# Performance work log

Hardware: AMD Instinct MI355X
Metric: run time of the kernel (lower is better)

The kernel has to match this reference:

```python
import jax, jax.numpy as jnp
import numpy as np

L, B, I, H = 1024, 128, 256, 512

def setup_inputs() -> dict:
    key = jax.random.key(0)
    k1, k2, k3, k4, k5 = jax.random.split(key, 5)
    s_i = 1.0 / np.sqrt(I)
    s_h = 1.0 / np.sqrt(H)
    return {
        "x": jax.random.normal(k1, (L, B, I), dtype=jnp.float32),
        "h": jax.random.normal(k2, (B, H), dtype=jnp.float32),
        "Wx": jax.random.uniform(k3, (H, I), jnp.float32, -s_i, s_i),
        "Wh": jax.random.uniform(k4, (H, H), jnp.float32, -s_h, s_h),
        "bh": jax.random.uniform(k5, (H,), jnp.float32, -s_h, s_h),
    }

def reference(x, h, Wx, Wh, bh):
    # Precompute input projection for all timesteps as one big GEMM:
    # (L,B,I) @ (I,H) -> (L,B,H)
    xproj = jnp.einsum("lbi,hi->lbh", x, Wx)

    def step(h_prev, xp_t):
        h_new = jnp.tanh(xp_t + h_prev @ Wh.T + bh)  # (B,H)
        return h_new, h_new

    _, h_seq = jax.lax.scan(step, h, xproj)
    return h_seq  # (L, B, H)
```

## Files before the change

### kernel.cpp

```cpp
#include <hip/hip_runtime.h>

#define L_DIM 1024
#define B_DIM 128
#define I_DIM 256
#define H_DIM 512

typedef unsigned short u16x8 __attribute__((ext_vector_type(8)));
typedef __bf16 bf16x8 __attribute__((ext_vector_type(8)));
typedef float f32x4 __attribute__((ext_vector_type(4)));
typedef unsigned long long u64;

static __device__ __forceinline__ unsigned short f2bf(float f) {
  unsigned u = __builtin_bit_cast(unsigned, f);
  u += 0x7FFFu + ((u >> 16) & 1u);
  return (unsigned short)(u >> 16);
}
static __device__ __forceinline__ float bf2f(unsigned short b) {
  return __builtin_bit_cast(float, ((unsigned)b) << 16);
}
static __device__ __forceinline__ bf16x8 ld_frag_g(const unsigned short* p, size_t idx8) {
  return __builtin_bit_cast(bf16x8, reinterpret_cast<const u16x8*>(p)[idx8]);
}

__global__ void pack_weights(const float* __restrict__ Wx, const float* __restrict__ Wh,
                             unsigned short* __restrict__ WxHi, unsigned short* __restrict__ WxLo,
                             unsigned short* __restrict__ WhHi, unsigned short* __restrict__ WhLo) {
  int tid = blockIdx.x * blockDim.x + threadIdx.x;
  if (tid < 32 * 8 * 64) {
    int lane = tid & 63, kt = (tid >> 6) & 7, nt = tid >> 9;
    int n = nt * 16 + (lane & 15), k0 = kt * 32 + (lane >> 4) * 8;
    const float* src = Wx + (size_t)n * I_DIM + k0;
    #pragma unroll
    for (int j = 0; j < 8; ++j) {
      float v = src[j];
      unsigned short hb = f2bf(v);
      WxHi[(size_t)tid * 8 + j] = hb;
      WxLo[(size_t)tid * 8 + j] = f2bf(v - bf2f(hb));
    }
  }
  if (tid < 32 * 16 * 64) {
    int lane = tid & 63, kt = (tid >> 6) & 15, nt = tid >> 10;
    int n = nt * 16 + (lane & 15), k0 = kt * 32 + (lane >> 4) * 8;
    const float* src = Wh + (size_t)n * H_DIM + k0;
    #pragma unroll
    for (int j = 0; j < 8; ++j) {
      float v = src[j];
      unsigned short hb = f2bf(v);
      WhHi[(size_t)tid * 8 + j] = hb;
      WhLo[(size_t)tid * 8 + j] = f2bf(v - bf2f(hb));
    }
  }
}

__global__ __launch_bounds__(256) void xproj_kernel(const float* __restrict__ x,
    const unsigned short* __restrict__ WxHi, const unsigned short* __restrict__ WxLo,
    const float* __restrict__ bh, float* __restrict__ out) {
  __shared__ unsigned short ahi[128][40];
  __shared__ unsigned short alo[128][40];
  const int tid = threadIdx.x, lane = tid & 63, wid = tid >> 6;
  const int mbase = blockIdx.x * 128, cbase = blockIdx.y * 128;
  const int wrow = (wid >> 1) * 64, wcol = (wid & 1) * 64;
  f32x4 acc[4][4] = {};
  const int srow = tid >> 1, shalf = (tid & 1) * 16;

  for (int kt = 0; kt < 8; ++kt) {
    const f32x4* src = reinterpret_cast<const f32x4*>(
        x + (size_t)(mbase + srow) * I_DIM + kt * 32 + shalf);
    f32x4 v[4];
    v[0] = src[0]; v[1] = src[1]; v[2] = src[2]; v[3] = src[3];
    u16x8 hh[2], ll[2];
    #pragma unroll
    for (int q = 0; q < 2; ++q) {
      #pragma unroll
      for (int e = 0; e < 8; ++e) {
        float f = v[q * 2 + (e >> 2)][e & 3];
        unsigned short hb = f2bf(f);
        hh[q][e] = hb;
        ll[q][e] = f2bf(f - bf2f(hb));
      }
    }
    __syncthreads();
    *reinterpret_cast<u16x8*>(&ahi[srow][shalf]) = hh[0];
    *reinterpret_cast<u16x8*>(&ahi[srow][shalf + 8]) = hh[1];
    *reinterpret_cast<u16x8*>(&alo[srow][shalf]) = ll[0];
    *reinterpret_cast<u16x8*>(&alo[srow][shalf + 8]) = ll[1];
    __syncthreads();

    bf16x8 amh[4], aml[4];
    #pragma unroll
    for (int m = 0; m < 4; ++m) {
      amh[m] = __builtin_bit_cast(bf16x8, *reinterpret_cast<const u16x8*>(
          &ahi[wrow + m * 16 + (lane & 15)][(lane >> 4) * 8]));
      aml[m] = __builtin_bit_cast(bf16x8, *reinterpret_cast<const u16x8*>(
          &alo[wrow + m * 16 + (lane & 15)][(lane >> 4) * 8]));
    }
    bf16x8 bhh[4], bll[4];
    #pragma unroll
    for (int n = 0; n < 4; ++n) {
      int ntg = (cbase + wcol) / 16 + n;
      size_t idx = (size_t)(ntg * 8 + kt) * 64 + lane;
      bhh[n] = ld_frag_g(WxHi, idx);
      bll[n] = ld_frag_g(WxLo, idx);
    }
    #pragma unroll
    for (int m = 0; m < 4; ++m) {
      #pragma unroll
      for (int n = 0; n < 4; ++n) {
        acc[m][n] = __builtin_amdgcn_mfma_f32_16x16x32_bf16(amh[m], bhh[n], acc[m][n], 0, 0, 0);
        acc[m][n] = __builtin_amdgcn_mfma_f32_16x16x32_bf16(aml[m], bhh[n], acc[m][n], 0, 0, 0);
        acc[m][n] = __builtin_amdgcn_mfma_f32_16x16x32_bf16(amh[m], bll[n], acc[m][n], 0, 0, 0);
      }
    }
  }

  #pragma unroll
  for (int n = 0; n < 4; ++n) {
    int col = cbase + wcol + n * 16 + (lane & 15);
    float bv = bh[col];
    #pragma unroll
    for (int m = 0; m < 4; ++m) {
      int rg = mbase + wrow + m * 16 + ((lane >> 4) << 2);
      #pragma unroll
      for (int r = 0; r < 4; ++r)
        out[(size_t)(rg + r) * H_DIM + col] = acc[m][n][r] + bv;
    }
  }
}

__global__ __launch_bounds__(256, 1) void rnn_kernel(const float* __restrict__ h0,
    const unsigned short* __restrict__ WhHi, const unsigned short* __restrict__ WhLo,
    unsigned int* __restrict__ tags, u64* __restrict__ gbuf,
    float* __restrict__ out) {
  __shared__ unsigned short hb[16 * 520];
  const int tid = threadIdx.x, lane = tid & 63, w = tid >> 6;
  const int g = blockIdx.x & 7, c = blockIdx.x >> 3;

  bf16x8 wfh[16], wfl[16];
  #pragma unroll
  for (int kt = 0; kt < 16; ++kt) {
    size_t idx = (size_t)((c * 4 + w) * 16 + kt) * 64 + lane;
    wfh[kt] = ld_frag_g(WhHi, idx);
    wfl[kt] = ld_frag_g(WhLo, idx);
  }
  for (int i = tid; i < 1024; i += 256) {
    int row = i >> 6, col0 = (i & 63) * 8;
    const f32x4* s = reinterpret_cast<const f32x4*>(h0 + (size_t)(g * 16 + row) * H_DIM + col0);
    f32x4 v0 = s[0], v1 = s[1];
    u16x8 hv;
    #pragma unroll
    for (int e = 0; e < 4; ++e) { hv[e] = f2bf(v0[e]); hv[4 + e] = f2bf(v1[e]); }
    *reinterpret_cast<u16x8*>(&hb[row * 520 + col0]) = hv;
  }
  __syncthreads();

  const int arow = lane & 15;
  const int aoff = (lane >> 4) * 8;
  const int drow = (lane >> 4) * 4;
  const int gcol = c * 64 + w * 16 + (lane & 15);
  const int pslot = (w * 16 + (lane & 15)) * 4 + (lane >> 4);
  const int ccol = tid >> 2;
  const int crow0 = (tid & 3) * 4;

  f32x4 xpv;
  #pragma unroll
  for (int r = 0; r < 4; ++r)
    xpv[r] = out[(size_t)(g * 16 + drow + r) * H_DIM + gcol];

  for (int t = 0; t < L_DIM; ++t) {
    const size_t obase = ((size_t)t * B_DIM + g * 16) * H_DIM;

    bf16x8 af[16];
    #pragma unroll
    for (int kt = 0; kt < 16; ++kt)
      af[kt] = __builtin_bit_cast(bf16x8, *reinterpret_cast<const u16x8*>(
          &hb[arow * 520 + kt * 32 + aoff]));
    f32x4 a0 = {}, a1 = {}, a2 = {}, a3 = {};
    #pragma unroll
    for (int kt = 0; kt < 16; kt += 2) {
      a0 = __builtin_amdgcn_mfma_f32_16x16x32_bf16(af[kt], wfh[kt], a0, 0, 0, 0);
      a1 = __builtin_amdgcn_mfma_f32_16x16x32_bf16(af[kt], wfl[kt], a1, 0, 0, 0);
      a2 = __builtin_amdgcn_mfma_f32_16x16x32_bf16(af[kt + 1], wfh[kt + 1], a2, 0, 0, 0);
      a3 = __builtin_amdgcn_mfma_f32_16x16x32_bf16(af[kt + 1], wfl[kt + 1], a3, 0, 0, 0);
    }

    float hv[4]; unsigned short hu[4];
    #pragma unroll
    for (int r = 0; r < 4; ++r) {
      float z = a0[r] + a1[r] + a2[r] + a3[r] + xpv[r];
      float e = __expf(2.0f * z);
      hv[r] = 1.0f - 2.0f / (e + 1.0f);
      hu[r] = f2bf(hv[r]);
    }

    if (t < L_DIM - 1) {
      const unsigned buf = (t + 1) & 1;
      u64 pv = (u64)hu[0] | ((u64)hu[1] << 16) | ((u64)hu[2] << 32) | ((u64)hu[3] << 48);
      __hip_atomic_store(gbuf + (((size_t)(buf * 8 + g) * 8 + c) * 256 + pslot), pv,
                         __ATOMIC_RELAXED, __HIP_MEMORY_SCOPE_AGENT);
      __builtin_amdgcn_sched_barrier(0);
      asm volatile("s_waitcnt vmcnt(0)" ::: "memory");
      __builtin_amdgcn_sched_barrier(0);
      if (lane == 0)
        __hip_atomic_store(tags + ((size_t)((buf * 8 + g) * 8 + c)) * 4 + w,
                           (unsigned)(t + 1), __ATOMIC_RELAXED, __HIP_MEMORY_SCOPE_AGENT);

      #pragma unroll
      for (int r = 0; r < 4; ++r)
        out[obase + (size_t)(drow + r) * H_DIM + gcol] = hv[r];
      const size_t obn = ((size_t)(t + 1) * B_DIM + g * 16) * H_DIM;
      #pragma unroll
      for (int r = 0; r < 4; ++r)
        xpv[r] = out[obn + (size_t)(drow + r) * H_DIM + gcol];

      if (lane < 7) {
        int s = lane + (lane >= c ? 1 : 0);
        const unsigned int* tp = tags + ((size_t)((buf * 8 + g) * 8 + s)) * 4 + w;
        while (__hip_atomic_load(tp, __ATOMIC_RELAXED, __HIP_MEMORY_SCOPE_AGENT)
               < (unsigned)(t + 1)) {}
      }
      __builtin_amdgcn_sched_barrier(0);
      u64 pul[7];
      #pragma unroll
      for (int si = 0; si < 7; ++si) {
        int s = si + (si >= c ? 1 : 0);
        pul[si] = __hip_atomic_load(gbuf + (((size_t)(buf * 8 + g) * 8 + s) * 256 + tid),
                                    __ATOMIC_RELAXED, __HIP_MEMORY_SCOPE_AGENT);
      }
      __builtin_amdgcn_sched_barrier(0);
      __builtin_amdgcn_s_barrier();
      __builtin_amdgcn_sched_barrier(0);
      #pragma unroll
      for (int r = 0; r < 4; ++r)
        hb[(drow + r) * 520 + gcol] = hu[r];
      #pragma unroll
      for (int si = 0; si < 7; ++si) {
        int s = si + (si >= c ? 1 : 0);
        #pragma unroll
        for (int dr = 0; dr < 4; ++dr)
          hb[(crow0 + dr) * 520 + s * 64 + ccol] = (unsigned short)(pul[si] >> (16 * dr));
      }
      __builtin_amdgcn_sched_barrier(0);
      asm volatile("s_waitcnt lgkmcnt(0)" ::: "memory");
      __builtin_amdgcn_sched_barrier(0);
      __builtin_amdgcn_s_barrier();
      __builtin_amdgcn_sched_barrier(0);
    } else {
      #pragma unroll
      for (int r = 0; r < 4; ++r)
        out[obase + (size_t)(drow + r) * H_DIM + gcol] = hv[r];
    }
  }
}

extern "C" void kernel_launch(void* const* d_in, const int* in_sizes, int n_in,
                              void* d_out, int out_size, void* d_ws, size_t ws_size,
                              hipStream_t stream) {
  (void)in_sizes; (void)n_in; (void)out_size; (void)ws_size;
  const float* x  = (const float*)d_in[0];
  const float* h0 = (const float*)d_in[1];
  const float* Wx = (const float*)d_in[2];
  const float* Wh = (const float*)d_in[3];
  const float* bh = (const float*)d_in[4];
  float* out = (float*)d_out;

  unsigned short* WxHi = (unsigned short*)d_ws;
  unsigned short* WxLo = WxHi + 131072;
  unsigned short* WhHi = WxLo + 131072;
  unsigned short* WhLo = WhHi + 262144;
  unsigned int*   tags = (unsigned int*)((char*)d_ws + 1572864);
  u64*            gbuf = (u64*)((char*)d_ws + 1575936);

  hipMemsetAsync(tags, 0, 2048, stream);

  hipLaunchKernelGGL(pack_weights, dim3(128), dim3(256), 0, stream,
                     Wx, Wh, WxHi, WxLo, WhHi, WhLo);
  hipLaunchKernelGGL(xproj_kernel, dim3(1024, 4), dim3(256), 0, stream,
                     x, WxHi, WxLo, bh, out);
  hipLaunchKernelGGL(rnn_kernel, dim3(64), dim3(256), 0, stream,
                     h0, WhHi, WhLo, tags, gbuf, out);
}
```

Baseline: 3.002 ms.

## Embed step tags in exchanged hidden-state words and double-buffer LDS

Each step's cross-block exchange of hidden state now writes every bf16 value together with the step number in one 32-bit word. Consumers spin directly on the data words, so the separate tag array, the vmcnt drain before the flag store and the pre-write barrier are all gone. The LDS hidden-state buffer is double-buffered, so the next step's copy can be filled without waiting for the current reads to finish. In exchange, each block now reads the full 16x512 slab from global memory instead of only its peers' slices. The slab reuses the workspace region that held the packed Wx weights and relies on stale contents never matching a step tag.

Result: slower. 4.140 ms (+37.9%).

```diff
diff --git a/kernel.cpp b/kernel.cpp
--- a/kernel.cpp
+++ b/kernel.cpp
@@ -9,6 +9,7 @@
 typedef __bf16 bf16x8 __attribute__((ext_vector_type(8)));
 typedef float f32x4 __attribute__((ext_vector_type(4)));
 typedef unsigned long long u64;
+typedef unsigned int u32;
 
 static __device__ __forceinline__ unsigned short f2bf(float f) {
   unsigned u = __builtin_bit_cast(unsigned, f);
@@ -129,9 +130,8 @@
 
 __global__ __launch_bounds__(256, 1) void rnn_kernel(const float* __restrict__ h0,
     const unsigned short* __restrict__ WhHi, const unsigned short* __restrict__ WhLo,
-    unsigned int* __restrict__ tags, u64* __restrict__ gbuf,
-    float* __restrict__ out) {
-  __shared__ unsigned short hb[16 * 520];
+    u32* __restrict__ slab, float* __restrict__ out) {
+  __shared__ __attribute__((aligned(16))) unsigned short hb[2][16 * 520];
   const int tid = threadIdx.x, lane = tid & 63, w = tid >> 6;
   const int g = blockIdx.x & 7, c = blockIdx.x >> 3;
 
@@ -149,7 +149,7 @@
     u16x8 hv;
     #pragma unroll
     for (int e = 0; e < 4; ++e) { hv[e] = f2bf(v0[e]); hv[4 + e] = f2bf(v1[e]); }
-    *reinterpret_cast<u16x8*>(&hb[row * 520 + col0]) = hv;
+    *reinterpret_cast<u16x8*>(&hb[0][row * 520 + col0]) = hv;
   }
   __syncthreads();
 
@@ -157,9 +157,6 @@
   const int aoff = (lane >> 4) * 8;
   const int drow = (lane >> 4) * 4;
   const int gcol = c * 64 + w * 16 + (lane & 15);
-  const int pslot = (w * 16 + (lane & 15)) * 4 + (lane >> 4);
-  const int ccol = tid >> 2;
-  const int crow0 = (tid & 3) * 4;
 
   f32x4 xpv;
   #pragma unroll
@@ -168,12 +165,13 @@
 
   for (int t = 0; t < L_DIM; ++t) {
     const size_t obase = ((size_t)t * B_DIM + g * 16) * H_DIM;
+    const unsigned short* hbc = hb[t & 1];
 
     bf16x8 af[16];
     #pragma unroll
     for (int kt = 0; kt < 16; ++kt)
       af[kt] = __builtin_bit_cast(bf16x8, *reinterpret_cast<const u16x8*>(
-          &hb[arow * 520 + kt * 32 + aoff]));
+          &hbc[arow * 520 + kt * 32 + aoff]));
     f32x4 a0 = {}, a1 = {}, a2 = {}, a3 = {};
     #pragma unroll
     for (int kt = 0; kt < 16; kt += 2) {
@@ -193,16 +191,14 @@
     }
 
     if (t < L_DIM - 1) {
-      const unsigned buf = (t + 1) & 1;
-      u64 pv = (u64)hu[0] | ((u64)hu[1] << 16) | ((u64)hu[2] << 32) | ((u64)hu[3] << 48);
-      __hip_atomic_store(gbuf + (((size_t)(buf * 8 + g) * 8 + c) * 256 + pslot), pv,
-                         __ATOMIC_RELAXED, __HIP_MEMORY_SCOPE_AGENT);
-      __builtin_amdgcn_sched_barrier(0);
-      asm volatile("s_waitcnt vmcnt(0)" ::: "memory");
-      __builtin_amdgcn_sched_barrier(0);
-      if (lane == 0)
-        __hip_atomic_store(tags + ((size_t)((buf * 8 + g) * 8 + c)) * 4 + w,
-                           (unsigned)(t + 1), __ATOMIC_RELAXED, __HIP_MEMORY_SCOPE_AGENT);
+      const unsigned step = (unsigned)(t + 1);
+      u32* sg = slab + ((size_t)((step & 1) * 8 + g)) * 8192;
+      const unsigned cbits = step << 16;
+
+      #pragma unroll
+      for (int r = 0; r < 4; ++r)
+        __hip_atomic_store(&sg[(drow + r) * 512 + gcol], cbits | (u32)hu[r],
+                           __ATOMIC_RELAXED, __HIP_MEMORY_SCOPE_AGENT);
 
       #pragma unroll
       for (int r = 0; r < 4; ++r)
@@ -212,32 +208,25 @@
       for (int r = 0; r < 4; ++r)
         xpv[r] = out[obn + (size_t)(drow + r) * H_DIM + gcol];
 
-      if (lane < 7) {
-        int s = lane + (lane >= c ? 1 : 0);
-        const unsigned int* tp = tags + ((size_t)((buf * 8 + g) * 8 + s)) * 4 + w;
-        while (__hip_atomic_load(tp, __ATOMIC_RELAXED, __HIP_MEMORY_SCOPE_AGENT)
-               < (unsigned)(t + 1)) {}
-      }
-      __builtin_amdgcn_sched_barrier(0);
-      u64 pul[7];
-      #pragma unroll
-      for (int si = 0; si < 7; ++si) {
-        int s = si + (si >= c ? 1 : 0);
-        pul[si] = __hip_atomic_load(gbuf + (((size_t)(buf * 8 + g) * 8 + s) * 256 + tid),
+      u64* sp = reinterpret_cast<u64*>(sg);
+      u64 pv[16];
+      #pragma unroll
+      for (int row = 0; row < 16; ++row)
+        pv[row] = __hip_atomic_load(sp + row * 256 + tid,
                                     __ATOMIC_RELAXED, __HIP_MEMORY_SCOPE_AGENT);
-      }
-      __builtin_amdgcn_sched_barrier(0);
-      __builtin_amdgcn_s_barrier();
-      __builtin_amdgcn_sched_barrier(0);
-      #pragma unroll
-      for (int r = 0; r < 4; ++r)
-        hb[(drow + r) * 520 + gcol] = hu[r];
-      #pragma unroll
-      for (int si = 0; si < 7; ++si) {
-        int s = si + (si >= c ? 1 : 0);
-        #pragma unroll
-        for (int dr = 0; dr < 4; ++dr)
-          hb[(crow0 + dr) * 520 + s * 64 + ccol] = (unsigned short)(pul[si] >> (16 * dr));
+      const u64 expect = (u64)step * 0x0001000000010000ull;
+      #pragma unroll
+      for (int row = 0; row < 16; ++row) {
+        while ((pv[row] & 0xFFFF0000FFFF0000ull) != expect)
+          pv[row] = __hip_atomic_load(sp + row * 256 + tid,
+                                      __ATOMIC_RELAXED, __HIP_MEMORY_SCOPE_AGENT);
+      }
+
+      unsigned short* hbn = hb[(t + 1) & 1];
+      #pragma unroll
+      for (int row = 0; row < 16; ++row) {
+        u32 pk = (u32)(pv[row] & 0xFFFFull) | (u32)((pv[row] >> 16) & 0xFFFF0000ull);
+        *reinterpret_cast<u32*>(&hbn[row * 520 + 2 * tid]) = pk;
       }
       __builtin_amdgcn_sched_barrier(0);
       asm volatile("s_waitcnt lgkmcnt(0)" ::: "memory");
@@ -267,15 +256,12 @@
   unsigned short* WxLo = WxHi + 131072;
   unsigned short* WhHi = WxLo + 131072;
   unsigned short* WhLo = WhHi + 262144;
-  unsigned int*   tags = (unsigned int*)((char*)d_ws + 1572864);
-  u64*            gbuf = (u64*)((char*)d_ws + 1575936);
-
-  hipMemsetAsync(tags, 0, 2048, stream);
+  u32* slab = (u32*)d_ws;
 
   hipLaunchKernelGGL(pack_weights, dim3(128), dim3(256), 0, stream,
                      Wx, Wh, WxHi, WxLo, WhHi, WhLo);
   hipLaunchKernelGGL(xproj_kernel, dim3(1024, 4), dim3(256), 0, stream,
                      x, WxHi, WxLo, bh, out);
   hipLaunchKernelGGL(rnn_kernel, dim3(64), dim3(256), 0, stream,
-                     h0, WhHi, WhLo, tags, gbuf, out);
-}
+                     h0, WhHi, WhLo, slab, out);
+}
```

## Double-buffer hidden-state LDS tile to drop one barrier per timestep

Applied to the files above, without the earlier changes.

Splits the shared hidden-state buffer into two halves alternating by timestep, so new values can be written into the next buffer without first waiting for all waves to finish reading the current one. This removes one of the two workgroup barriers in each recurrent step. It also prefetches the input projection two steps ahead rather than one, to hide global load latency. In exchange it doubles LDS use and makes correctness depend on the ping-pong ordering across the remaining barrier.

Measured after the change: 2.804 ms. 6.6% less time.

```diff
diff --git a/kernel.cpp b/kernel.cpp
--- a/kernel.cpp
+++ b/kernel.cpp
@@ -9,6 +9,7 @@
 typedef __bf16 bf16x8 __attribute__((ext_vector_type(8)));
 typedef float f32x4 __attribute__((ext_vector_type(4)));
 typedef unsigned long long u64;
+typedef unsigned int u32;
 
 static __device__ __forceinline__ unsigned short f2bf(float f) {
   unsigned u = __builtin_bit_cast(unsigned, f);
@@ -131,7 +132,7 @@
     const unsigned short* __restrict__ WhHi, const unsigned short* __restrict__ WhLo,
     unsigned int* __restrict__ tags, u64* __restrict__ gbuf,
     float* __restrict__ out) {
-  __shared__ unsigned short hb[16 * 520];
+  __shared__ unsigned short hb[2][16 * 520];
   const int tid = threadIdx.x, lane = tid & 63, w = tid >> 6;
   const int g = blockIdx.x & 7, c = blockIdx.x >> 3;
 
@@ -149,7 +150,7 @@
     u16x8 hv;
     #pragma unroll
     for (int e = 0; e < 4; ++e) { hv[e] = f2bf(v0[e]); hv[4 + e] = f2bf(v1[e]); }
-    *reinterpret_cast<u16x8*>(&hb[row * 520 + col0]) = hv;
+    *reinterpret_cast<u16x8*>(&hb[0][row * 520 + col0]) = hv;
   }
   __syncthreads();
 
@@ -161,19 +162,23 @@
   const int ccol = tid >> 2;
   const int crow0 = (tid & 3) * 4;
 
-  f32x4 xpv;
+  f32x4 xpA, xpB;
   #pragma unroll
   for (int r = 0; r < 4; ++r)
-    xpv[r] = out[(size_t)(g * 16 + drow + r) * H_DIM + gcol];
+    xpA[r] = out[(size_t)(g * 16 + drow + r) * H_DIM + gcol];
+  #pragma unroll
+  for (int r = 0; r < 4; ++r)
+    xpB[r] = out[(size_t)B_DIM * H_DIM + (size_t)(g * 16 + drow + r) * H_DIM + gcol];
 
   for (int t = 0; t < L_DIM; ++t) {
     const size_t obase = ((size_t)t * B_DIM + g * 16) * H_DIM;
+    const int cur = t & 1;
 
     bf16x8 af[16];
     #pragma unroll
     for (int kt = 0; kt < 16; ++kt)
       af[kt] = __builtin_bit_cast(bf16x8, *reinterpret_cast<const u16x8*>(
-          &hb[arow * 520 + kt * 32 + aoff]));
+          &hb[cur][arow * 520 + kt * 32 + aoff]));
     f32x4 a0 = {}, a1 = {}, a2 = {}, a3 = {};
     #pragma unroll
     for (int kt = 0; kt < 16; kt += 2) {
@@ -186,69 +191,74 @@
     float hv[4]; unsigned short hu[4];
     #pragma unroll
     for (int r = 0; r < 4; ++r) {
-      float z = a0[r] + a1[r] + a2[r] + a3[r] + xpv[r];
+      float z = a0[r] + a1[r] + a2[r] + a3[r] + xpA[r];
       float e = __expf(2.0f * z);
       hv[r] = 1.0f - 2.0f / (e + 1.0f);
       hu[r] = f2bf(hv[r]);
     }
 
-    if (t < L_DIM - 1) {
-      const unsigned buf = (t + 1) & 1;
-      u64 pv = (u64)hu[0] | ((u64)hu[1] << 16) | ((u64)hu[2] << 32) | ((u64)hu[3] << 48);
-      __hip_atomic_store(gbuf + (((size_t)(buf * 8 + g) * 8 + c) * 256 + pslot), pv,
-                         __ATOMIC_RELAXED, __HIP_MEMORY_SCOPE_AGENT);
-      __builtin_amdgcn_sched_barrier(0);
-      asm volatile("s_waitcnt vmcnt(0)" ::: "memory");
-      __builtin_amdgcn_sched_barrier(0);
-      if (lane == 0)
-        __hip_atomic_store(tags + ((size_t)((buf * 8 + g) * 8 + c)) * 4 + w,
-                           (unsigned)(t + 1), __ATOMIC_RELAXED, __HIP_MEMORY_SCOPE_AGENT);
-
+    if (t == L_DIM - 1) {
       #pragma unroll
       for (int r = 0; r < 4; ++r)
         out[obase + (size_t)(drow + r) * H_DIM + gcol] = hv[r];
-      const size_t obn = ((size_t)(t + 1) * B_DIM + g * 16) * H_DIM;
+      break;
+    }
+
+    const unsigned step = (unsigned)(t + 1);
+    const unsigned buf = step & 1;
+
+    u64 pv = (u64)hu[0] | ((u64)hu[1] << 16) | ((u64)hu[2] << 32) | ((u64)hu[3] << 48);
+    __hip_atomic_store(gbuf + (((size_t)(buf * 8 + g) * 8 + c) * 256 + pslot), pv,
+                       __ATOMIC_RELAXED, __HIP_MEMORY_SCOPE_AGENT);
+    __builtin_amdgcn_sched_barrier(0);
+    asm volatile("s_waitcnt vmcnt(0)" ::: "memory");
+    __builtin_amdgcn_sched_barrier(0);
+    if (lane == 0)
+      __hip_atomic_store(tags + ((size_t)((buf * 8 + g) * 8 + c)) * 4 + w,
+                         step, __ATOMIC_RELAXED, __HIP_MEMORY_SCOPE_AGENT);
+
+    #pragma unroll
+    for (int r = 0; r < 4; ++r)
+      hb[buf][(drow + r) * 520 + gcol] = hu[r];
+
+    #pragma unroll
+    for (int r = 0; r < 4; ++r)
+      out[obase + (size_t)(drow + r) * H_DIM + gcol] = hv[r];
+    xpA = xpB;
+    {
+      const int tn = (t + 2 < L_DIM) ? t + 2 : L_DIM - 1;
+      const size_t obn = ((size_t)tn * B_DIM + g * 16) * H_DIM;
       #pragma unroll
       for (int r = 0; r < 4; ++r)
-        xpv[r] = out[obn + (size_t)(drow + r) * H_DIM + gcol];
-
-      if (lane < 7) {
-        int s = lane + (lane >= c ? 1 : 0);
-        const unsigned int* tp = tags + ((size_t)((buf * 8 + g) * 8 + s)) * 4 + w;
-        while (__hip_atomic_load(tp, __ATOMIC_RELAXED, __HIP_MEMORY_SCOPE_AGENT)
-               < (unsigned)(t + 1)) {}
-      }
-      __builtin_amdgcn_sched_barrier(0);
-      u64 pul[7];
-      #pragma unroll
-      for (int si = 0; si < 7; ++si) {
-        int s = si + (si >= c ? 1 : 0);
-        pul[si] = __hip_atomic_load(gbuf + (((size_t)(buf * 8 + g) * 8 + s) * 256 + tid),
-                                    __ATOMIC_RELAXED, __HIP_MEMORY_SCOPE_AGENT);
-      }
-      __builtin_amdgcn_sched_barrier(0);
-      __builtin_amdgcn_s_barrier();
-      __builtin_amdgcn_sched_barrier(0);
-      #pragma unroll
-      for (int r = 0; r < 4; ++r)
-        hb[(drow + r) * 520 + gcol] = hu[r];
-      #pragma unroll
-      for (int si = 0; si < 7; ++si) {
-        int s = si + (si >= c ? 1 : 0);
-        #pragma unroll
-        for (int dr = 0; dr < 4; ++dr)
-          hb[(crow0 + dr) * 520 + s * 64 + ccol] = (unsigned short)(pul[si] >> (16 * dr));
-      }
-      __builtin_amdgcn_sched_barrier(0);
-      asm volatile("s_waitcnt lgkmcnt(0)" ::: "memory");
-      __builtin_amdgcn_sched_barrier(0);
-      __builtin_amdgcn_s_barrier();
-      __builtin_amdgcn_sched_barrier(0);
-    } else {
-      #pragma unroll
-      for (int r = 0; r < 4; ++r)
-        out[obase + (size_t)(drow + r) * H_DIM + gcol] = hv[r];
-    }
+        xpB[r] = out[obn + (size_t)(drow + r) * H_DIM + gcol];
+    }
+
+    if (lane < 7) {
+      int s = lane + (lane >= c ? 1 : 0);
+      const unsigned int* tp = tags + ((size_t)((buf * 8 + g) * 8 + s)) * 4 + w;
+      while (__hip_atomic_load(tp, __ATOMIC_RELAXED, __HIP_MEMORY_SCOPE_AGENT) < step) {}
+    }
+    __builtin_amdgcn_sched_barrier(0);
+    u64 pul[7];
+    #pragma unroll
+    for (int si = 0; si < 7; ++si) {
+      int s = si + (si >= c ? 1 : 0);
+      pul[si] = __hip_atomic_load(gbuf + (((size_t)(buf * 8 + g) * 8 + s) * 256 + tid),
+                                  __ATOMIC_RELAXED, __HIP_MEMORY_SCOPE_AGENT);
+    }
+    __builtin_amdgcn_sched_barrier(0);
+    #pragma unroll
+    for (int si = 0; si < 7; ++si) {
+      int s = si + (si >= c ? 1 : 0);
+      #pragma unroll
+      for (int dr = 0; dr < 4; ++dr)
+        hb[buf][(crow0 + dr) * 520 + s * 64 + ccol] = (unsigned short)(pul[si] >> (16 * dr));
+    }
+    __builtin_amdgcn_sched_barrier(0);
+    asm volatile("s_waitcnt lgkmcnt(0)" ::: "memory");
+    __builtin_amdgcn_sched_barrier(0);
+    __builtin_amdgcn_s_barrier();
+    __builtin_amdgcn_sched_barrier(0);
   }
 }
 
```
